# Kernel optimization log

Hardware: AMD Instinct MI355X
Metric: run time of the kernel (lower is better)

Reference implementation:

```python
import jax, jax.numpy as jnp
import numpy as np

B, C_IN, C_OUT, H, W = 4, 64, 64, 64, 64
D = 2 * C_OUT  # projected channel dim = 128


def conv1x1(x, w, b):
    # x: [B,Cin,H,W], w: [Cout,Cin], b: [Cout]
    return jnp.einsum('bchw,oc->bohw', x, w) + b[None, :, None, None]


def setup_inputs() -> dict:
    key = jax.random.key(0)
    ks = jax.random.split(key, 10)
    s_q = 1.0 / np.sqrt(C_IN)
    s_kv = 1.0 / np.sqrt(2 * C_IN)
    s_o = 1.0 / np.sqrt(D)
    return {
        'x_upper': jax.random.normal(ks[0], (B, C_IN, H, W), jnp.float32),
        'x_lower': jax.random.normal(ks[1], (B, 2 * C_IN, H, W), jnp.float32),
        'wq': jax.random.uniform(ks[2], (D, C_IN), jnp.float32, -s_q, s_q),
        'bq': jax.random.uniform(ks[3], (D,), jnp.float32, -s_q, s_q),
        'wk': jax.random.uniform(ks[4], (D, 2 * C_IN), jnp.float32, -s_kv, s_kv),
        'bk': jax.random.uniform(ks[5], (D,), jnp.float32, -s_kv, s_kv),
        'wv': jax.random.uniform(ks[6], (D, 2 * C_IN), jnp.float32, -s_kv, s_kv),
        'bv': jax.random.uniform(ks[7], (D,), jnp.float32, -s_kv, s_kv),
        'wo': jax.random.uniform(ks[8], (D, D), jnp.float32, -s_o, s_o),
        'bo': jax.random.uniform(ks[9], (D,), jnp.float32, -s_o, s_o),
    }


def reference(x_upper, x_lower, wq, bq, wk, bk, wv, bv, wo, bo):
    q = conv1x1(x_upper, wq, bq)   # [B,D,H,W]
    k = conv1x1(x_lower, wk, bk)   # [B,D,H,W]
    v = conv1x1(x_lower, wv, bv)   # [B,D,H,W]
    b, d = q.shape[0], q.shape[1]
    # NOTE: the torch code uses .view (raw reshape), NOT a transpose --
    # faithful translation is a plain reshape of the contiguous NCHW tensor.
    qf = q.reshape(b, -1, d)       # [B, N, D], N = H*W
    kf = k.reshape(b, -1, d)
    vf = v.reshape(b, -1, d)
    scores = jnp.einsum('bnd,bmd->bnm', qf, kf) / (d ** 0.5)  # [B,N,N]
    attn = jax.nn.softmax(scores, axis=-1)
    of = jnp.einsum('bnm,bmd->bnd', attn, vf)  # [B,N,D]
    out = of.reshape(v.shape)                  # [B,D,H,W]
    out = conv1x1(out, wo, bo) + x_lower
    return out
```

## Files before the change

### kernel.cpp

```cpp
#include <hip/hip_runtime.h>
#include <math.h>

#define BB 4
#define CIN 64
#define CL 128
#define DD 128
#define HW 4096
#define NN 4096
#define TP 132
#define YP 136

typedef __attribute__((ext_vector_type(8))) __bf16 bf16x8;
typedef __attribute__((ext_vector_type(16))) float f32x16;

__device__ __forceinline__ unsigned short f2bf(float f) {
    unsigned u = __builtin_bit_cast(unsigned, f);
    u += 0x7fffu + ((u >> 16) & 1u);
    return (unsigned short)(u >> 16);
}
__device__ __forceinline__ unsigned pack2(float lo, float hi) {
    return (unsigned)f2bf(lo) | ((unsigned)f2bf(hi) << 16);
}
__device__ __forceinline__ float bf2f(unsigned s) {
    return __builtin_bit_cast(float, s << 16);
}
__device__ __forceinline__ unsigned pack_trunc(float lo, float hi) {
    return __builtin_amdgcn_perm(__builtin_bit_cast(unsigned, hi),
                                 __builtin_bit_cast(unsigned, lo), 0x07060302u);
}
__device__ __forceinline__ float exp2_fast(float x) {
#if __has_builtin(__builtin_amdgcn_exp2f)
    return __builtin_amdgcn_exp2f(x);
#else
    return __expf(x * 0.6931471805599453f);
#endif
}
__device__ __forceinline__ void async_copy16(const unsigned short* g,
                                             unsigned short* l) {
    __builtin_amdgcn_global_load_lds(
        (const __attribute__((address_space(1))) void*)g,
        (__attribute__((address_space(3))) void*)l, 16, 0, 0);
}

__device__ __forceinline__ void split8(const float xv[8], bf16x8* hi, bf16x8* lo) {
    union { unsigned u[4]; bf16x8 v; } H, L;
#pragma unroll
    for (int i = 0; i < 4; ++i) {
        float x0 = xv[2 * i], x1 = xv[2 * i + 1];
        H.u[i] = pack_trunc(x0, x1);
        float h0 = __builtin_bit_cast(float,
                     __builtin_bit_cast(unsigned, x0) & 0xffff0000u);
        float h1 = __builtin_bit_cast(float,
                     __builtin_bit_cast(unsigned, x1) & 0xffff0000u);
        L.u[i] = pack_trunc(x0 - h0, x1 - h1);
    }
    *hi = H.v; *lo = L.v;
}


__global__ __launch_bounds__(512) void proj_qkv_mfma(
    const float* __restrict__ xq, const float* __restrict__ wq,
    const float* __restrict__ bq, unsigned short* __restrict__ qout,
    const float* __restrict__ xl,
    const float* __restrict__ wk, const float* __restrict__ bk,
    const float* __restrict__ wv, const float* __restrict__ bv,
    unsigned short* __restrict__ kout, unsigned short* __restrict__ vout,
    float oscale)
{
    __shared__ __align__(16) char smem[135168];
    float* xsf = (float*)smem;
    unsigned short* ytk = (unsigned short*)(smem + 65536);
    unsigned short* ytv = (unsigned short*)(smem + 100352);

    const int tid = threadIdx.x;
    const int w = tid >> 6;
    const int lane = tid & 63;
    const int half = lane >> 5;
    const int l5 = lane & 31;

    if (blockIdx.x < 128) {
        const int b = blockIdx.x >> 5;
        const int tile = blockIdx.x & 31;
        const int px0 = tile * 128;
        const int g = w >> 2;
        const int ms = w & 3;

        {
            const float* src = xl + (size_t)b * CL * HW + px0
                             + (size_t)(lane >> 5) * HW + (lane & 31) * 4;
#pragma unroll
            for (int k = 0; k < 8; ++k) {
                int c = w * 8 + k;
                async_copy16((const unsigned short*)(src + (size_t)(2 * c) * HW),
                             (unsigned short*)(smem + c * 1024));
            }
        }

        const float* wsrc = g ? wv : wk;
        const float* bsrc = g ? bv : bk;
        bf16x8 Ah[8], Al[8];
        {
            const float* wr = wsrc + (size_t)(ms * 32 + l5) * CL + half * 8;
#pragma unroll
            for (int ks = 0; ks < 8; ++ks) {
                float tmp[8];
                *(float4*)&tmp[0] = *(const float4*)(wr + ks * 16);
                *(float4*)&tmp[4] = *(const float4*)(wr + ks * 16 + 4);
                split8(tmp, &Ah[ks], &Al[ks]);
            }
        }
        float biasr[16];
#pragma unroll
        for (int r = 0; r < 16; ++r)
            biasr[r] = bsrc[ms * 32 + (r & 3) + 8 * (r >> 2) + 4 * half];

        f32x16 acc[4];
#pragma unroll
        for (int ns = 0; ns < 4; ++ns)
#pragma unroll
            for (int r = 0; r < 16; ++r) acc[ns][r] = biasr[r];

        asm volatile("s_waitcnt vmcnt(0)" ::: "memory");
        __builtin_amdgcn_s_barrier();
        asm volatile("" ::: "memory");

#pragma unroll
        for (int ns = 0; ns < 4; ++ns) {
            int pxl = ns * 32 + l5;
#pragma unroll
            for (int ks = 0; ks < 8; ++ks) {
                int kb_ = ks * 16 + half * 8;
                float xv[8];
#pragma unroll
                for (int j = 0; j < 8; ++j)
                    xv[j] = xsf[(kb_ + j) * 128 + pxl];
                bf16x8 Bh, Bl;
                split8(xv, &Bh, &Bl);
                acc[ns] = __builtin_amdgcn_mfma_f32_32x32x16_bf16(Ah[ks], Bh, acc[ns], 0, 0, 0);
                acc[ns] = __builtin_amdgcn_mfma_f32_32x32x16_bf16(Ah[ks], Bl, acc[ns], 0, 0, 0);
                acc[ns] = __builtin_amdgcn_mfma_f32_32x32x16_bf16(Al[ks], Bh, acc[ns], 0, 0, 0);
            }
        }

        unsigned short* yt = g ? ytv : ytk;
#pragma unroll
        for (int ns = 0; ns < 4; ++ns) {
            int pxl = ns * 32 + l5;
#pragma unroll
            for (int r = 0; r < 16; ++r) {
                int o = ms * 32 + (r & 3) + 8 * (r >> 2) + 4 * half;
                yt[o * YP + pxl] = f2bf(acc[ns][r]);
            }
        }
        __syncthreads();

        unsigned short* kbase = kout + (size_t)b * NN * DD;
        unsigned short* vbase = vout + (size_t)b * 128 * HW + px0;
        const int tm = tile & 15;
#pragma unroll
        for (int i = 0; i < 4; ++i) {
            int e = tid + i * 512;
            int o = e >> 4, q = e & 15;
            uint4 kq4 = *(const uint4*)(ytk + o * YP + q * 8);
            *(uint4*)(kbase + (size_t)(o * 32 + tile) * 128 + ((q ^ tm) * 8)) = kq4;
            uint4 vq4 = *(const uint4*)(ytv + o * YP + q * 8);
            *(uint4*)(vbase + (size_t)o * HW + q * 8) = vq4;
        }
    } else {
        const int qb_ = blockIdx.x - 128;
        const int b = qb_ >> 5;
        const int tile = qb_ & 31;
        const int px0 = tile * 128;
        const int ms = w & 3;
        const int nsg = w >> 2;

        {
            const float* src = xq + (size_t)b * CIN * HW + px0
                             + (size_t)(lane >> 5) * HW + (lane & 31) * 4;
#pragma unroll
            for (int k = 0; k < 4; ++k) {
                int c = w * 4 + k;
                async_copy16((const unsigned short*)(src + (size_t)(2 * c) * HW),
                             (unsigned short*)(smem + c * 1024));
            }
        }

        bf16x8 Ah[4], Al[4];
        {
            const float* wr = wq + (size_t)(ms * 32 + l5) * CIN + half * 8;
#pragma unroll
            for (int ks = 0; ks < 4; ++ks) {
                float tmp[8];
                *(float4*)&tmp[0] = *(const float4*)(wr + ks * 16);
                *(float4*)&tmp[4] = *(const float4*)(wr + ks * 16 + 4);
                split8(tmp, &Ah[ks], &Al[ks]);
            }
        }
        float biasr[16];
#pragma unroll
        for (int r = 0; r < 16; ++r)
            biasr[r] = bq[ms * 32 + (r & 3) + 8 * (r >> 2) + 4 * half];

        f32x16 acc[2];
#pragma unroll
        for (int i = 0; i < 2; ++i)
#pragma unroll
            for (int r = 0; r < 16; ++r) acc[i][r] = biasr[r];

        asm volatile("s_waitcnt vmcnt(0)" ::: "memory");
        __builtin_amdgcn_s_barrier();
        asm volatile("" ::: "memory");

#pragma unroll
        for (int i = 0; i < 2; ++i) {
            int pxl = (nsg * 2 + i) * 32 + l5;
#pragma unroll
            for (int ks = 0; ks < 4; ++ks) {
                int kb_ = ks * 16 + half * 8;
                float xv[8];
#pragma unroll
                for (int j = 0; j < 8; ++j)
                    xv[j] = xsf[(kb_ + j) * 128 + pxl];
                bf16x8 Bh, Bl;
                split8(xv, &Bh, &Bl);
                acc[i] = __builtin_amdgcn_mfma_f32_32x32x16_bf16(Ah[ks], Bh, acc[i], 0, 0, 0);
                acc[i] = __builtin_amdgcn_mfma_f32_32x32x16_bf16(Ah[ks], Bl, acc[i], 0, 0, 0);
                acc[i] = __builtin_amdgcn_mfma_f32_32x32x16_bf16(Al[ks], Bh, acc[i], 0, 0, 0);
            }
        }

#pragma unroll
        for (int i = 0; i < 2; ++i) {
            int pxl = (nsg * 2 + i) * 32 + l5;
#pragma unroll
            for (int r = 0; r < 16; ++r) {
                int o = ms * 32 + (r & 3) + 8 * (r >> 2) + 4 * half;
                ytk[o * YP + pxl] = f2bf(acc[i][r] * oscale);
            }
        }
        __syncthreads();

        unsigned short* qbase = qout + (size_t)b * 128 * HW + px0;
#pragma unroll
        for (int i = 0; i < 4; ++i) {
            int e = tid + i * 512;
            int o = e >> 4, q = e & 15;
            uint4 qq4 = *(const uint4*)(ytk + o * YP + q * 8);
            *(uint4*)(qbase + (size_t)o * HW + q * 8) = qq4;
        }
    }
}

__global__ __launch_bounds__(512) void proj_o_mfma(
    const unsigned short* __restrict__ x, const float* __restrict__ w,
    const float* __restrict__ bias, const float* __restrict__ resid,
    float* __restrict__ out)
{
    __shared__ __align__(16) unsigned short xs16[128 * 128];

    const int tid = threadIdx.x;
    const int w_ = tid >> 6;
    const int lane = tid & 63;
    const int half = lane >> 5;
    const int l5 = lane & 31;
    const int b = blockIdx.x >> 5;
    const int tile = blockIdx.x & 31;
    const int px0 = tile * 128;
    const int ms = w_ & 3;
    const int nsg = w_ >> 2;

    {
        const unsigned short* src = x + (size_t)b * DD * HW + px0
                                  + (size_t)(lane >> 4) * HW + (lane & 15) * 8;
#pragma unroll
        for (int k = 0; k < 4; ++k) {
            int c = w_ * 4 + k;
            async_copy16(src + (size_t)(4 * c) * HW, xs16 + c * 512);
        }
    }

    bf16x8 Ah[8], Al[8];
    {
        const float* wr = w + (size_t)(ms * 32 + l5) * DD + half * 8;
#pragma unroll
        for (int ks = 0; ks < 8; ++ks) {
            float tmp[8];
            *(float4*)&tmp[0] = *(const float4*)(wr + ks * 16);
            *(float4*)&tmp[4] = *(const float4*)(wr + ks * 16 + 4);
            split8(tmp, &Ah[ks], &Al[ks]);
        }
    }
    float biasr[16];
#pragma unroll
    for (int r = 0; r < 16; ++r)
        biasr[r] = bias[ms * 32 + (r & 3) + 8 * (r >> 2) + 4 * half];

    f32x16 acc[2];
#pragma unroll
    for (int i = 0; i < 2; ++i)
#pragma unroll
        for (int r = 0; r < 16; ++r) acc[i][r] = biasr[r];

    asm volatile("s_waitcnt vmcnt(0)" ::: "memory");
    __builtin_amdgcn_s_barrier();
    asm volatile("" ::: "memory");

#pragma unroll
    for (int i = 0; i < 2; ++i) {
        int pxl = (nsg * 2 + i) * 32 + l5;
#pragma unroll
        for (int ks = 0; ks < 8; ++ks) {
            int kb_ = ks * 16 + half * 8;
            union { unsigned u[4]; bf16x8 v; } B;
#pragma unroll
            for (int p = 0; p < 4; ++p) {
                unsigned e0 = xs16[(kb_ + 2 * p) * 128 + pxl];
                unsigned e1 = xs16[(kb_ + 2 * p + 1) * 128 + pxl];
                B.u[p] = e0 | (e1 << 16);
            }
            acc[i] = __builtin_amdgcn_mfma_f32_32x32x16_bf16(Ah[ks], B.v, acc[i], 0, 0, 0);
            acc[i] = __builtin_amdgcn_mfma_f32_32x32x16_bf16(Al[ks], B.v, acc[i], 0, 0, 0);
        }
    }

#pragma unroll
    for (int i = 0; i < 2; ++i) {
        int px = px0 + (nsg * 2 + i) * 32 + l5;
#pragma unroll
        for (int r = 0; r < 16; ++r) {
            int o = ms * 32 + (r & 3) + 8 * (r >> 2) + 4 * half;
            size_t a = ((size_t)b * 128 + o) * HW + px;
            out[a] = acc[i][r] + resid[a];
        }
    }
}

__global__ __launch_bounds__(256) void transpose_v(
    const unsigned short* __restrict__ vf, unsigned short* __restrict__ vt)
{
    __shared__ unsigned short tld[64 * TP];
    int tid = threadIdx.x;
    int b = blockIdx.x >> 6;
    int n0 = (blockIdx.x & 63) * 64;
    const unsigned short* src = vf + (size_t)b * NN * DD + (size_t)n0 * DD;
#pragma unroll
    for (int i = 0; i < 4; ++i) {
        int ch = tid + i * 256;
        int n = ch >> 4, x = ch & 15;
        union { uint4 q; unsigned long long u[2]; } t;
        t.q = *(const uint4*)(src + (size_t)n * DD + x * 8);
        unsigned short* d = &tld[n * TP + x * 8];
        *(unsigned long long*)(d) = t.u[0];
        *(unsigned long long*)(d + 4) = t.u[1];
    }
    __syncthreads();
    unsigned short* dst = vt + (size_t)b * NN * DD + (size_t)(n0 >> 7) * 16384;
    int xb_ = (n0 & 127) >> 3;
#pragma unroll
    for (int i = 0; i < 4; ++i) {
        int ch = tid + i * 256;
        int g = ch & 7, d = ch >> 3;
        union { uint4 q; unsigned short s[8]; } t;
#pragma unroll
        for (int j = 0; j < 8; ++j) t.s[j] = tld[(g * 8 + j) * TP + d];
        int xs = (xb_ + g) ^ (d & 15);
        *(uint4*)(dst + (size_t)d * 128 + xs * 8) = t.q;
    }
}

__global__ __launch_bounds__(512) void attn_mfma(
    const unsigned short* __restrict__ qf, const unsigned short* __restrict__ kfs,
    const unsigned short* __restrict__ vts, unsigned short* __restrict__ of)
{
    __shared__ __align__(16) char smem[133632];

    const int tid = threadIdx.x;
    const int lane = tid & 63;
    const int w = tid >> 6;
    const int kq = w & 3;
    const int rh = w >> 2;
    const int half = lane >> 5;
    const int l5 = lane & 31;
    const int b = blockIdx.x >> 6;
    const int rb0 = (blockIdx.x & 63) * 64;
    const int rw0 = rb0 + rh * 32;
    const int cw = kq * 32;

    const unsigned short* qb = qf + (size_t)b * NN * DD;
    const unsigned short* kb = kfs + (size_t)b * NN * DD;
    const unsigned short* vb = vts + (size_t)b * NN * DD;

    bf16x8 qfrag[8];
    {
        const unsigned short* qrow = qb + (size_t)(rw0 + l5) * DD + half * 8;
#pragma unroll
        for (int kk = 0; kk < 8; ++kk)
            qfrag[kk] = *(const bf16x8*)(qrow + kk * 16);
    }

    f32x16 O[4] = {};
    float lacc = 0.f;

    auto stage = [&](int t, int buf) {
        const unsigned short* kt = kb + (size_t)t * 16384;
        const unsigned short* vt_ = vb + (size_t)t * 16384;
        unsigned short* kl = (unsigned short*)(smem + buf * 65536);
        unsigned short* vl = kl + 16384;
#pragma unroll
        for (int j = 0; j < 4; ++j) {
            int c = (w * 4 + j) * 512;
            async_copy16(kt + c + lane * 8, kl + c);
            async_copy16(vt_ + c + lane * 8, vl + c);
        }
    };

    stage(0, 0);
    stage(1, 1);

    const int NT = NN / 128;
    for (int t = 0; t < NT; ++t) {
        const int cur = t & 1;
        if (t < NT - 1) asm volatile("s_waitcnt vmcnt(8)" ::: "memory");
        else            asm volatile("s_waitcnt vmcnt(0)" ::: "memory");
        __builtin_amdgcn_s_barrier();
        asm volatile("" ::: "memory");

        const unsigned short* kl = (const unsigned short*)(smem + cur * 65536);
        const unsigned short* vl = kl + 16384;

        f32x16 S = {};
#pragma unroll
        for (int kk = 0; kk < 8; ++kk) {
            bf16x8 kfr = *(const bf16x8*)
                &kl[(cw + l5) * 128 + (((kk * 2 + half) ^ (l5 & 15)) * 8)];
            S = __builtin_amdgcn_mfma_f32_32x32x16_bf16(kfr, qfrag[kk], S, 0, 0, 0);
        }

        float p[16];
#pragma unroll
        for (int r = 0; r < 16; ++r) p[r] = exp2_fast(S[r]);
        {
            float t0 = (p[0] + p[1]) + (p[2] + p[3]);
            float t1 = (p[4] + p[5]) + (p[6] + p[7]);
            float t2 = (p[8] + p[9]) + (p[10] + p[11]);
            float t3 = (p[12] + p[13]) + (p[14] + p[15]);
            lacc += (t0 + t1) + (t2 + t3);
        }

#pragma unroll
        for (int kc = 0; kc < 2; ++kc) {
            unsigned PA0 = pack_trunc(p[8 * kc + 0], p[8 * kc + 1]);
            unsigned PA1 = pack_trunc(p[8 * kc + 2], p[8 * kc + 3]);
            unsigned PB0 = pack_trunc(p[8 * kc + 4], p[8 * kc + 5]);
            unsigned PB1 = pack_trunc(p[8 * kc + 6], p[8 * kc + 7]);
            unsigned snd0 = half ? PA0 : PB0;
            unsigned snd1 = half ? PA1 : PB1;
            unsigned rcv0 = (unsigned)__shfl_xor((int)snd0, 32, 64);
            unsigned rcv1 = (unsigned)__shfl_xor((int)snd1, 32, 64);
            union { unsigned u[4]; bf16x8 v; } pf;
            pf.u[0] = half ? rcv0 : PA0;
            pf.u[1] = half ? rcv1 : PA1;
            pf.u[2] = half ? PB0 : rcv0;
            pf.u[3] = half ? PB1 : rcv1;
#pragma unroll
            for (int ds = 0; ds < 4; ++ds) {
                bf16x8 vfr = *(const bf16x8*)
                    &vl[(ds * 32 + l5) * 128 +
                        (((kq * 4 + kc * 2 + half) ^ (l5 & 15)) * 8)];
                O[ds] = __builtin_amdgcn_mfma_f32_32x32x16_bf16(vfr, pf.v, O[ds], 0, 0, 0);
            }
        }

        asm volatile("s_waitcnt lgkmcnt(0)" ::: "memory");
        __builtin_amdgcn_s_barrier();
        asm volatile("" ::: "memory");
        if (t + 2 < NT) stage(t + 2, cur);
    }

    lacc += __shfl_xor(lacc, 32, 64);

    float (*red_o)[64][129] = (float (*)[64][129])smem;
    float* red_l = (float*)(smem + 132096);
    if (half == 0) red_l[kq * 64 + rh * 32 + l5] = lacc;
#pragma unroll
    for (int ds = 0; ds < 4; ++ds)
#pragma unroll
        for (int r = 0; r < 16; ++r) {
            int d = ds * 32 + (r & 3) + 8 * (r >> 2) + 4 * half;
            red_o[kq][rh * 32 + l5][d] = O[ds][r];
        }
    __syncthreads();

    {
        int q = tid >> 3;
        int dg = tid & 7;
        float l = red_l[q] + red_l[64 + q] + red_l[128 + q] + red_l[192 + q];
        float inv = 1.f / l;
        unsigned outw[8];
#pragma unroll
        for (int i = 0; i < 8; ++i) {
            int d0 = dg * 16 + i * 2;
            float s0 = red_o[0][q][d0] + red_o[1][q][d0] +
                       red_o[2][q][d0] + red_o[3][q][d0];
            float s1 = red_o[0][q][d0 + 1] + red_o[1][q][d0 + 1] +
                       red_o[2][q][d0 + 1] + red_o[3][q][d0 + 1];
            outw[i] = pack2(s0 * inv, s1 * inv);
        }
        unsigned short* ob = of + (size_t)b * NN * DD + (size_t)(rb0 + q) * DD + dg * 16;
        *(uint4*)(ob) = *(uint4*)&outw[0];
        *(uint4*)(ob + 8) = *(uint4*)&outw[4];
    }
}

extern "C" void kernel_launch(void* const* d_in, const int* in_sizes, int n_in,
                              void* d_out, int out_size, void* d_ws, size_t ws_size,
                              hipStream_t stream) {
    const float* x_upper = (const float*)d_in[0];
    const float* x_lower = (const float*)d_in[1];
    const float* wq = (const float*)d_in[2];
    const float* bq = (const float*)d_in[3];
    const float* wk = (const float*)d_in[4];
    const float* bk = (const float*)d_in[5];
    const float* wv = (const float*)d_in[6];
    const float* bv = (const float*)d_in[7];
    const float* wo = (const float*)d_in[8];
    const float* bo = (const float*)d_in[9];
    float* out = (float*)d_out;

    const size_t ELT = (size_t)BB * NN * DD;
    unsigned short* qf  = (unsigned short*)d_ws;
    unsigned short* kfs = qf + ELT;
    unsigned short* vts = kfs + ELT;
    unsigned short* vfn = vts + ELT;
    unsigned short* ofb = vfn + ELT;

    const float qscale = (float)(0.08838834764831845 * 1.4426950408889634);

    proj_qkv_mfma<<<256, 512, 0, stream>>>(x_upper, wq, bq, qf,
                                           x_lower, wk, bk, wv, bv,
                                           kfs, vfn, qscale);
    transpose_v<<<256, 256, 0, stream>>>(vfn, vts);
    attn_mfma<<<BB * 64, 512, 0, stream>>>(qf, kfs, vts, ofb);
    proj_o_mfma<<<128, 512, 0, stream>>>(ofb, wo, bo, x_lower, out);
}
```

Before: 153.9 us.

## Shrink proj_o and transpose tiles for more blocks; add setprio around MFMA

Output projection now processes 64 pixels per block, so 256 blocks are launched instead of 128. The V transpose handles 16 rows per block, so 1024 blocks are launched instead of 256. The attention kernel wraps its MFMA loops in s_setprio raise/lower to favour waves issuing matrix ops. The goal is better CU occupancy on the small kernels and better interleaving in attention, at the cost of less per-block reuse of the weight splits in proj_o and more block launch overhead.

```diff
diff --git a/kernel.cpp b/kernel.cpp
--- a/kernel.cpp
+++ b/kernel.cpp
@@ -56,7 +56,6 @@
     }
     *hi = H.v; *lo = L.v;
 }
-
 
 __global__ __launch_bounds__(512) void proj_qkv_mfma(
     const float* __restrict__ xq, const float* __restrict__ wq,
@@ -256,26 +255,26 @@
     const float* __restrict__ bias, const float* __restrict__ resid,
     float* __restrict__ out)
 {
-    __shared__ __align__(16) unsigned short xs16[128 * 128];
+    __shared__ __align__(16) unsigned short xs16[128 * 64];
 
     const int tid = threadIdx.x;
     const int w_ = tid >> 6;
     const int lane = tid & 63;
     const int half = lane >> 5;
     const int l5 = lane & 31;
-    const int b = blockIdx.x >> 5;
-    const int tile = blockIdx.x & 31;
-    const int px0 = tile * 128;
+    const int b = blockIdx.x >> 6;
+    const int tile = blockIdx.x & 63;
+    const int px0 = tile * 64;
     const int ms = w_ & 3;
-    const int nsg = w_ >> 2;
+    const int pxh = w_ >> 2;
 
     {
         const unsigned short* src = x + (size_t)b * DD * HW + px0
-                                  + (size_t)(lane >> 4) * HW + (lane & 15) * 8;
-#pragma unroll
-        for (int k = 0; k < 4; ++k) {
-            int c = w_ * 4 + k;
-            async_copy16(src + (size_t)(4 * c) * HW, xs16 + c * 512);
+                                  + (size_t)(lane >> 3) * HW + (lane & 7) * 8;
+#pragma unroll
+        for (int k = 0; k < 2; ++k) {
+            int c = w_ * 2 + k;
+            async_copy16(src + (size_t)(8 * c) * HW, xs16 + c * 512);
         }
     }
 
@@ -290,47 +289,39 @@
             split8(tmp, &Ah[ks], &Al[ks]);
         }
     }
-    float biasr[16];
+    f32x16 acc;
 #pragma unroll
     for (int r = 0; r < 16; ++r)
-        biasr[r] = bias[ms * 32 + (r & 3) + 8 * (r >> 2) + 4 * half];
-
-    f32x16 acc[2];
-#pragma unroll
-    for (int i = 0; i < 2; ++i)
-#pragma unroll
-        for (int r = 0; r < 16; ++r) acc[i][r] = biasr[r];
+        acc[r] = bias[ms * 32 + (r & 3) + 8 * (r >> 2) + 4 * half];
 
     asm volatile("s_waitcnt vmcnt(0)" ::: "memory");
     __builtin_amdgcn_s_barrier();
     asm volatile("" ::: "memory");
 
-#pragma unroll
-    for (int i = 0; i < 2; ++i) {
-        int pxl = (nsg * 2 + i) * 32 + l5;
+    {
+        int pxl = pxh * 32 + l5;
 #pragma unroll
         for (int ks = 0; ks < 8; ++ks) {
             int kb_ = ks * 16 + half * 8;
             union { unsigned u[4]; bf16x8 v; } B;
 #pragma unroll
             for (int p = 0; p < 4; ++p) {
-                unsigned e0 = xs16[(kb_ + 2 * p) * 128 + pxl];
-                unsigned e1 = xs16[(kb_ + 2 * p + 1) * 128 + pxl];
+                unsigned e0 = xs16[(kb_ + 2 * p) * 64 + pxl];
+                unsigned e1 = xs16[(kb_ + 2 * p + 1) * 64 + pxl];
                 B.u[p] = e0 | (e1 << 16);
             }
-            acc[i] = __builtin_amdgcn_mfma_f32_32x32x16_bf16(Ah[ks], B.v, acc[i], 0, 0, 0);
-            acc[i] = __builtin_amdgcn_mfma_f32_32x32x16_bf16(Al[ks], B.v, acc[i], 0, 0, 0);
-        }
-    }
-
-#pragma unroll
-    for (int i = 0; i < 2; ++i) {
-        int px = px0 + (nsg * 2 + i) * 32 + l5;
+            acc = __builtin_amdgcn_mfma_f32_32x32x16_bf16(Ah[ks], B.v, acc, 0, 0, 0);
+            acc = __builtin_amdgcn_mfma_f32_32x32x16_bf16(Al[ks], B.v, acc, 0, 0, 0);
+        }
+    }
+
+    {
+        int px = px0 + pxh * 32 + l5;
 #pragma unroll
         for (int r = 0; r < 16; ++r) {
             int o = ms * 32 + (r & 3) + 8 * (r >> 2) + 4 * half;
             size_t a = ((size_t)b * 128 + o) * HW + px;
-            out[a] = acc[i][r] + resid[a];
+            out[a] = acc[r] + resid[a];
         }
     }
 }
@@ -338,15 +329,13 @@
 __global__ __launch_bounds__(256) void transpose_v(
     const unsigned short* __restrict__ vf, unsigned short* __restrict__ vt)
 {
-    __shared__ unsigned short tld[64 * TP];
+    __shared__ unsigned short tld[16 * TP];
     int tid = threadIdx.x;
-    int b = blockIdx.x >> 6;
-    int n0 = (blockIdx.x & 63) * 64;
+    int b = blockIdx.x >> 8;
+    int n0 = (blockIdx.x & 255) * 16;
     const unsigned short* src = vf + (size_t)b * NN * DD + (size_t)n0 * DD;
-#pragma unroll
-    for (int i = 0; i < 4; ++i) {
-        int ch = tid + i * 256;
-        int n = ch >> 4, x = ch & 15;
+    {
+        int n = tid >> 4, x = tid & 15;
         union { uint4 q; unsigned long long u[2]; } t;
         t.q = *(const uint4*)(src + (size_t)n * DD + x * 8);
         unsigned short* d = &tld[n * TP + x * 8];
@@ -356,10 +345,8 @@
     __syncthreads();
     unsigned short* dst = vt + (size_t)b * NN * DD + (size_t)(n0 >> 7) * 16384;
     int xb_ = (n0 & 127) >> 3;
-#pragma unroll
-    for (int i = 0; i < 4; ++i) {
-        int ch = tid + i * 256;
-        int g = ch & 7, d = ch >> 3;
+    {
+        int g = tid & 1, d = tid >> 1;
         union { uint4 q; unsigned short s[8]; } t;
 #pragma unroll
         for (int j = 0; j < 8; ++j) t.s[j] = tld[(g * 8 + j) * TP + d];
@@ -429,12 +416,14 @@
         const unsigned short* vl = kl + 16384;
 
         f32x16 S = {};
+        __builtin_amdgcn_s_setprio(1);
 #pragma unroll
         for (int kk = 0; kk < 8; ++kk) {
             bf16x8 kfr = *(const bf16x8*)
                 &kl[(cw + l5) * 128 + (((kk * 2 + half) ^ (l5 & 15)) * 8)];
             S = __builtin_amdgcn_mfma_f32_32x32x16_bf16(kfr, qfrag[kk], S, 0, 0, 0);
         }
+        __builtin_amdgcn_s_setprio(0);
 
         float p[16];
 #pragma unroll
@@ -462,6 +451,7 @@
             pf.u[1] = half ? rcv1 : PA1;
             pf.u[2] = half ? PB0 : rcv0;
             pf.u[3] = half ? PB1 : rcv1;
+            __builtin_amdgcn_s_setprio(1);
 #pragma unroll
             for (int ds = 0; ds < 4; ++ds) {
                 bf16x8 vfr = *(const bf16x8*)
@@ -469,6 +459,7 @@
                         (((kq * 4 + kc * 2 + half) ^ (l5 & 15)) * 8)];
                 O[ds] = __builtin_amdgcn_mfma_f32_32x32x16_bf16(vfr, pf.v, O[ds], 0, 0, 0);
             }
+            __builtin_amdgcn_s_setprio(0);
         }
 
         asm volatile("s_waitcnt lgkmcnt(0)" ::: "memory");
@@ -539,7 +530,7 @@
     proj_qkv_mfma<<<256, 512, 0, stream>>>(x_upper, wq, bq, qf,
                                            x_lower, wk, bk, wv, bv,
                                            kfs, vfn, qscale);
-    transpose_v<<<256, 256, 0, stream>>>(vfn, vts);
+    transpose_v<<<1024, 256, 0, stream>>>(vfn, vts);
     attn_mfma<<<BB * 64, 512, 0, stream>>>(qf, kfs, vts, ofb);
-    proj_o_mfma<<<128, 512, 0, stream>>>(ofb, wo, bo, x_lower, out);
-}
+    proj_o_mfma<<<256, 512, 0, stream>>>(ofb, wo, bo, x_lower, out);
+}
```

Result: faster. 150.3 us (-2.3%).
